# Kernel tuning notes

Measured on AMD Instinct MI355X. Metric: run time of the kernel, lower is better.

## Reference

```python
import jax, jax.numpy as jnp
import numpy as np
from itertools import product

D = 128        # input voxel grid side
N_IN = 150000  # active input voxels
C_IN = 32
C_OUT = 64
M = 100000     # active output voxels kept after stride-2 downsample
EPS = 1e-5


def _build_rulebooks():
    rng = np.random.default_rng(0)
    flat = rng.choice(D ** 3, size=N_IN, replace=False)
    coords = np.stack(np.unravel_index(flat, (D, D, D)), axis=1).astype(np.int64)  # [N_IN,3]
    # SparseConv3d(kernel=2, stride=2, padding=1): input i contributes to output o with
    # i = 2*o - 1 + k, k in {0,1}; per dim exactly one k is valid -> o = (i+1)//2.
    out_all = (coords + 1) // 2
    koff = (coords + 1) % 2
    kidx = koff[:, 0] * 4 + koff[:, 1] * 2 + koff[:, 2]
    out_coords, inv = np.unique(out_all, axis=0, return_inverse=True)
    assert len(out_coords) >= M, 'not enough occupied parent voxels'
    out_coords = out_coords[:M]
    nbr_down = -np.ones((M, 8), np.int32)
    sel = inv < M
    nbr_down[inv[sel], kidx[sel]] = np.arange(N_IN, dtype=np.int32)[sel]
    # SubMConv3d(kernel=3, padding=1): output sites == input sites; neighbor table per offset.
    S = 67  # hash stride (out coords in [0,65), +1 shift keeps neighbor keys in range)
    key = (out_coords[:, 0] + 1) * S * S + (out_coords[:, 1] + 1) * S + (out_coords[:, 2] + 1)
    lut = -np.ones(S ** 3, np.int32)
    lut[key] = np.arange(M, dtype=np.int32)
    nbr_sub = np.empty((M, 27), np.int32)
    for k, (dx, dy, dz) in enumerate(product((-1, 0, 1), repeat=3)):
        nbr_sub[:, k] = lut[key + dx * S * S + dy * S + dz]
    return nbr_down, nbr_sub


def setup_inputs() -> dict:
    nbr_down, nbr_sub = _build_rulebooks()
    key = jax.random.key(0)
    k0, k1, k2, k3, k4 = jax.random.split(key, 5)
    ones = jnp.ones((C_OUT,), jnp.float32)
    zeros = jnp.zeros((C_OUT,), jnp.float32)
    return {
        'x_feats': jax.random.normal(k0, (N_IN, C_IN), jnp.float32),
        'w_down': jax.random.normal(k1, (8, C_IN, C_OUT), jnp.float32) / np.sqrt(8 * C_IN),
        'g_down': ones, 'b_down': zeros,
        'w_proj': jax.random.normal(k2, (C_OUT, C_OUT), jnp.float32) / np.sqrt(C_OUT),
        'g_p': ones, 'b_p': zeros,
        'w1': jax.random.normal(k3, (27, C_OUT, C_OUT), jnp.float32) / np.sqrt(27 * C_OUT),
        'g1': ones, 'b1': zeros,
        'w2': jax.random.normal(k4, (27, C_OUT, C_OUT), jnp.float32) / np.sqrt(27 * C_OUT),
        'g2': ones, 'b2': zeros,
        'nbr_down': jnp.asarray(nbr_down),
        'nbr_sub': jnp.asarray(nbr_sub),
    }


def _bn(f, g, b):
    # BatchNorm1d in training mode over the active-voxel dim (biased variance)
    m = f.mean(0)
    v = jnp.mean((f - m) ** 2, 0)
    return (f - m) * jax.lax.rsqrt(v + EPS) * g + b


def _spconv(feats, nbr, W):
    # rulebook gather-GEMM-scatter: out[m] = sum_k feats[nbr[m,k]] @ W[k]  (nbr=-1 -> zero)
    n = feats.shape[0]
    fpad = jnp.concatenate([feats, jnp.zeros((1, feats.shape[1]), feats.dtype)], axis=0)
    idx = jnp.where(nbr < 0, n, nbr)
    out = jnp.zeros((nbr.shape[0], W.shape[2]), feats.dtype)
    for k in range(W.shape[0]):  # fixed small kernel volume (8 or 27)
        out = out + fpad[idx[:, k]] @ W[k]
    return out


def reference(x_feats, w_down, g_down, b_down, w_proj, g_p, b_p,
              w1, g1, b1, w2, g2, b2, nbr_down, nbr_sub):
    # DonwBlock.down: SparseConv3d -> BN -> ReLU
    x = jax.nn.relu(_bn(_spconv(x_feats, nbr_down, w_down), g_down, b_down))
    # DoubleConv.proj: 1x1 SubMConv (plain linear on features) -> BN
    res = _bn(x @ w_proj, g_p, b_p)
    # conv1 -> bn1 -> relu -> conv2 -> bn2 -> +proj -> relu
    out = jax.nn.relu(_bn(_spconv(x, nbr_sub, w1), g1, b1))
    out = _bn(_spconv(out, nbr_sub, w2), g2, b2) + res
    return jax.nn.relu(out)
```

## Files before the change

### kernel.cpp

```cpp
#include <hip/hip_runtime.h>

static constexpr int M_ROWS = 100000;
static constexpr int N_IN   = 150000;
static constexpr int C_IN   = 32;
static constexpr int CO     = 64;
static constexpr float EPS  = 1e-5f;

typedef __bf16 bf16x8 __attribute__((ext_vector_type(8)));
typedef float  f32x4  __attribute__((ext_vector_type(4)));
typedef unsigned short u16x8 __attribute__((ext_vector_type(8)));
typedef short  short8 __attribute__((ext_vector_type(8)));
typedef unsigned int u32;

static __device__ __forceinline__ unsigned short f2bf(float f) {
    unsigned int u = __builtin_bit_cast(unsigned int, f);
    u += 0x7fff + ((u >> 16) & 1);
    return (unsigned short)(u >> 16);
}
static __device__ __forceinline__ float bf2f(unsigned short h) {
    unsigned int u = ((unsigned int)h) << 16;
    return __builtin_bit_cast(float, u);
}

static __device__ __forceinline__ void gload_lds16(const void* g, void* l) {
    __builtin_amdgcn_global_load_lds(
        (const __attribute__((address_space(1))) u32*)g,
        (__attribute__((address_space(3))) u32*)l, 16, 0, 0);
}

__global__ __launch_bounds__(256) void cvt_bf16(
    const float* __restrict__ in, unsigned short* __restrict__ out, int n8)
{
    int i = blockIdx.x * 256 + threadIdx.x;
    if (i >= n8) return;
    float4 a = ((const float4*)in)[2 * i];
    float4 b = ((const float4*)in)[2 * i + 1];
    u16x8 v;
    v[0] = f2bf(a.x); v[1] = f2bf(a.y); v[2] = f2bf(a.z); v[3] = f2bf(a.w);
    v[4] = f2bf(b.x); v[5] = f2bf(b.y); v[6] = f2bf(b.z); v[7] = f2bf(b.w);
    ((u16x8*)out)[i] = v;
}

__global__ __launch_bounds__(256) void wt_cvt_swz(
    const float* __restrict__ W, unsigned short* __restrict__ WT, int total, int cin)
{
    int t = blockIdx.x * 256 + threadIdx.x;
    if (t >= total) return;
    int k  = t / (cin * 64);
    int r  = t - k * (cin * 64);
    int ci = r >> 6;
    int co = r & 63;
    int xm = (cin == 64) ? ((co & 7) << 4) : ((co & 3) << 4);
    int phys = co * (cin * 2) + ((ci * 2) ^ xm);
    WT[(size_t)k * cin * 64 + (phys >> 1)] = f2bf(W[t]);
}

template<int CIN, int KOFF, int ST, bool GATHER, bool OUTBF>
__global__ __launch_bounds__(256, 2) void spconv_mfma(
    const unsigned short* __restrict__ fB,
    int nZero,
    const int*   __restrict__ nbr,
    const unsigned short* __restrict__ WTs,
    void* __restrict__ outp,
    float* __restrict__ part)
{
    constexpr int KS    = CIN / 32;
    constexpr int SLAB  = CIN * 64;
    constexpr int REPS  = (SLAB * 2) / 4096;
    constexpr int ROWSB = 4 * ST * 16;

    __shared__ unsigned short Wl[2][SLAB];
    __shared__ int nbrS[GATHER ? ROWSB * KOFF : 4];
    __shared__ float red[4][2][64];

    const int tid  = threadIdx.x;
    const int lane = tid & 63;
    const int wv   = tid >> 6;
    const int colb = lane & 15;
    const int kgrp = lane >> 4;

    const int nwg = gridDim.x;
    const int q   = nwg >> 3, r8 = nwg & 7;
    const int xcd = blockIdx.x & 7, pos = blockIdx.x >> 3;
    const int wg  = (xcd < r8 ? xcd * (q + 1) : r8 * (q + 1) + (xcd - r8) * q) + pos;
    const int m0  = wg * ROWSB;

    auto stageW = [&](int k, int b) {
        const unsigned short* g = WTs + (size_t)k * SLAB;
        #pragma unroll
        for (int r = 0; r < REPS; ++r) {
            const void* gp = g + (size_t)(r * 256 + tid) * 8;
            void* lp = &Wl[b][(size_t)(r * 256 + wv * 64) * 8];
            gload_lds16(gp, lp);
        }
    };

    stageW(0, 0);
    if (GATHER) {
        const int* src = nbr + (size_t)m0 * KOFF;
        constexpr int TOT = ROWSB * KOFF;
        if (m0 + ROWSB <= M_ROWS) {
            #pragma unroll 1
            for (int i = tid; i < TOT / 4; i += 256)
                ((int4*)nbrS)[i] = ((const int4*)src)[i];
        } else {
            #pragma unroll 1
            for (int i = tid; i < TOT; i += 256) {
                int r = i / KOFF;
                nbrS[i] = (m0 + r < M_ROWS) ? src[i] : -1;
            }
        }
    }
    __syncthreads();

    auto gatherA = [&](int k, bf16x8 (&dst)[ST][KS]) {
        #pragma unroll
        for (int st = 0; st < ST; ++st) {
            int rloc = wv * (ST * 16) + st * 16 + colb;
            int idx;
            if (GATHER) idx = nbrS[rloc * KOFF + k];
            else        idx = (m0 + rloc < M_ROWS) ? (m0 + rloc) : -1;
            if (idx < 0) idx = nZero;
            const unsigned short* fp = fB + (size_t)idx * CIN + kgrp * 8;
            #pragma unroll
            for (int s = 0; s < KS; ++s)
                dst[st][s] = *reinterpret_cast<const bf16x8*>(fp + s * 32);
        }
    };

    f32x4 acc[ST][4] = {};

    auto compute = [&](int buf, const bf16x8 (&a)[ST][KS]) {
        bf16x8 w[4][KS];
        const char* base = (const char*)&Wl[0][0] + (size_t)buf * SLAB * 2;
        #pragma unroll
        for (int n = 0; n < 4; ++n) {
            int r  = n * 16 + colb;
            int xm = (CIN == 64) ? ((r & 7) << 4) : ((r & 3) << 4);
            #pragma unroll
            for (int s = 0; s < KS; ++s) {
                int c2 = kgrp * 16 + s * 64;
                int phys = r * (CIN * 2) + (c2 ^ xm);
                w[n][s] = *reinterpret_cast<const bf16x8*>(base + phys);
            }
        }
        #pragma unroll
        for (int st = 0; st < ST; ++st)
            #pragma unroll
            for (int n = 0; n < 4; ++n)
                #pragma unroll
                for (int s = 0; s < KS; ++s)
                    acc[st][n] = __builtin_amdgcn_mfma_f32_16x16x32_bf16(
                        a[st][s], w[n][s], acc[st][n], 0, 0, 0);
    };

    #pragma unroll 1
    for (int k = 0; k < KOFF; ++k) {
        bf16x8 a[ST][KS];
        gatherA(k, a);
        if (k + 1 < KOFF) stageW(k + 1, (k + 1) & 1);
        compute(k & 1, a);
        if (k + 1 < KOFF) __syncthreads();
    }

    #pragma unroll
    for (int st = 0; st < ST; ++st) {
        int rbase = m0 + wv * (ST * 16) + st * 16 + kgrp * 4;
        #pragma unroll
        for (int j = 0; j < 4; ++j) {
            int row = rbase + j;
            if (row < M_ROWS) {
                if (OUTBF) {
                    unsigned short* o = (unsigned short*)outp;
                    #pragma unroll
                    for (int n = 0; n < 4; ++n)
                        o[(size_t)row * 64 + n * 16 + colb] = f2bf(acc[st][n][j]);
                } else {
                    float* o = (float*)outp;
                    #pragma unroll
                    for (int n = 0; n < 4; ++n)
                        o[(size_t)row * 64 + n * 16 + colb] = acc[st][n][j];
                }
            }
        }
    }

    float s4[4], q4[4];
    #pragma unroll
    for (int n = 0; n < 4; ++n) {
        float s = 0.f, qq = 0.f;
        #pragma unroll
        for (int st = 0; st < ST; ++st)
            #pragma unroll
            for (int j = 0; j < 4; ++j) {
                float v = acc[st][n][j];
                s += v; qq += v * v;
            }
        s4[n] = s; q4[n] = qq;
    }
    #pragma unroll
    for (int n = 0; n < 4; ++n) {
        s4[n] += __shfl_xor(s4[n], 16); s4[n] += __shfl_xor(s4[n], 32);
        q4[n] += __shfl_xor(q4[n], 16); q4[n] += __shfl_xor(q4[n], 32);
    }
    if (kgrp == 0) {
        #pragma unroll
        for (int n = 0; n < 4; ++n) {
            red[wv][0][n * 16 + colb] = s4[n];
            red[wv][1][n * 16 + colb] = q4[n];
        }
    }
    __syncthreads();
    if (tid < 64) {
        float S = red[0][0][tid] + red[1][0][tid] + red[2][0][tid] + red[3][0][tid];
        float Q = red[0][1][tid] + red[1][1][tid] + red[2][1][tid] + red[3][1][tid];
        part[(size_t)wg * 128 + tid]      = S;
        part[(size_t)wg * 128 + 64 + tid] = Q;
    }
}

__global__ __launch_bounds__(1024) void bn_finalize(
    const float* __restrict__ part, int nblocks,
    const float* __restrict__ gg, const float* __restrict__ bb,
    float* __restrict__ ss, int M)
{
    const int tid = threadIdx.x;
    const int c   = tid & 63;
    const int grp = tid >> 6;
    float S = 0.f, Q = 0.f;
    int i = grp;
    for (; i + 48 < nblocks; i += 64) {
        float a0 = part[(size_t)(i     ) * 128 + c];
        float a1 = part[(size_t)(i + 16) * 128 + c];
        float a2 = part[(size_t)(i + 32) * 128 + c];
        float a3 = part[(size_t)(i + 48) * 128 + c];
        float q0 = part[(size_t)(i     ) * 128 + 64 + c];
        float q1 = part[(size_t)(i + 16) * 128 + 64 + c];
        float q2 = part[(size_t)(i + 32) * 128 + 64 + c];
        float q3 = part[(size_t)(i + 48) * 128 + 64 + c];
        S += a0 + a1 + a2 + a3;
        Q += q0 + q1 + q2 + q3;
    }
    for (; i < nblocks; i += 16) {
        S += part[(size_t)i * 128 + c];
        Q += part[(size_t)i * 128 + 64 + c];
    }
    __shared__ float sh[2][16][64];
    sh[0][grp][c] = S; sh[1][grp][c] = Q;
    __syncthreads();
    if (tid < 64) {
        float Sa = 0.f, Qa = 0.f;
        #pragma unroll
        for (int j = 0; j < 16; ++j) { Sa += sh[0][j][tid]; Qa += sh[1][j][tid]; }
        float mean = Sa / (float)M;
        float var  = Qa / (float)M - mean * mean;
        float rstd = rsqrtf(var + EPS);
        float sc = gg[tid] * rstd;
        ss[tid]      = sc;
        ss[64 + tid] = bb[tid] - mean * sc;
    }
}

template<bool INBF, bool BF16OUT, bool RES, bool RELU>
__global__ __launch_bounds__(256) void bn_apply(
    const void* __restrict__ yp, const float* __restrict__ ss,
    const unsigned short* __restrict__ res, void* __restrict__ out, int n8)
{
    for (int i = blockIdx.x * 256 + threadIdx.x; i < n8; i += gridDim.x * 256) {
        float v[8];
        if (INBF) {
            u16x8 u = ((const u16x8*)yp)[i];
            #pragma unroll
            for (int j = 0; j < 8; ++j) v[j] = bf2f(u[j]);
        } else {
            float4 a = ((const float4*)yp)[2 * i];
            float4 b = ((const float4*)yp)[2 * i + 1];
            v[0] = a.x; v[1] = a.y; v[2] = a.z; v[3] = a.w;
            v[4] = b.x; v[5] = b.y; v[6] = b.z; v[7] = b.w;
        }
        int c0 = (i * 8) & 63;
        #pragma unroll
        for (int j = 0; j < 8; ++j)
            v[j] = v[j] * ss[c0 + j] + ss[64 + c0 + j];
        if (RES) {
            u16x8 rv = ((const u16x8*)res)[i];
            #pragma unroll
            for (int j = 0; j < 8; ++j) v[j] += bf2f(rv[j]);
        }
        if (RELU) {
            #pragma unroll
            for (int j = 0; j < 8; ++j) v[j] = fmaxf(v[j], 0.f);
        }
        if (BF16OUT) {
            u16x8 o;
            #pragma unroll
            for (int j = 0; j < 8; ++j) o[j] = f2bf(v[j]);
            ((u16x8*)out)[i] = o;
        } else {
            float4 oa, ob;
            oa.x = v[0]; oa.y = v[1]; oa.z = v[2]; oa.w = v[3];
            ob.x = v[4]; ob.y = v[5]; ob.z = v[6]; ob.w = v[7];
            ((float4*)out)[2 * i]     = oa;
            ((float4*)out)[2 * i + 1] = ob;
        }
    }
}

extern "C" void kernel_launch(void* const* d_in, const int* in_sizes, int n_in,
                              void* d_out, int out_size, void* d_ws, size_t ws_size,
                              hipStream_t stream)
{
    const float* x_feats = (const float*)d_in[0];
    const float* w_down  = (const float*)d_in[1];
    const float* g_down  = (const float*)d_in[2];
    const float* b_down  = (const float*)d_in[3];
    const float* w_proj  = (const float*)d_in[4];
    const float* g_p     = (const float*)d_in[5];
    const float* b_p     = (const float*)d_in[6];
    const float* w1      = (const float*)d_in[7];
    const float* g1      = (const float*)d_in[8];
    const float* b1      = (const float*)d_in[9];
    const float* w2      = (const float*)d_in[10];
    const float* g2      = (const float*)d_in[11];
    const float* b2      = (const float*)d_in[12];
    const int*   nbr_down = (const int*)d_in[13];
    const int*   nbr_sub  = (const int*)d_in[14];
    float* out = (float*)d_out;

    const int M = M_ROWS;
    const int conv_grid = (M + 255) / 256;
    const size_t feat4 = (size_t)M * CO * 4;
    const size_t feat2 = (size_t)(M + 1) * CO * 2;
    auto align = [](size_t x) { return (x + 255) & ~(size_t)255; };

    char* ws = (char*)d_ws;
    size_t off = 0;
    unsigned short* xin16 = (unsigned short*)(ws + off); off += align((size_t)(N_IN + 1) * C_IN * 2);
    unsigned short* wdT   = (unsigned short*)(ws + off); off += align((size_t)8 * CO * C_IN * 2);
    unsigned short* wpT   = (unsigned short*)(ws + off); off += align((size_t)1 * CO * CO * 2);
    unsigned short* w1T   = (unsigned short*)(ws + off); off += align((size_t)27 * CO * CO * 2);
    unsigned short* w2T   = (unsigned short*)(ws + off); off += align((size_t)27 * CO * CO * 2);
    float* Y    = (float*)(ws + off); off += align(feat4);
    unsigned short* bufRb = (unsigned short*)(ws + off); off += align(feat2);
    unsigned short* xB = (unsigned short*)(ws + off); off += align(feat2);
    unsigned short* zB = (unsigned short*)(ws + off); off += align(feat2);
    float* part = (float*)(ws + off); off += align((size_t)1024 * 128 * 4);
    float* ss0  = (float*)(ws + off);
    float* ss1  = ss0 + 128;
    float* ss2  = ss1 + 128;
    float* ss3  = ss2 + 128;

    unsigned short* Yb = (unsigned short*)Y;

    const int n8 = M * CO / 8;
    const int ew_grid = 2048;

    hipMemsetAsync(xin16 + (size_t)N_IN * C_IN, 0, C_IN * 2, stream);
    hipMemsetAsync(xB + (size_t)M * CO, 0, CO * 2, stream);
    hipMemsetAsync(zB + (size_t)M * CO, 0, CO * 2, stream);

    {
        int nf8 = N_IN * C_IN / 8;
        cvt_bf16<<<(nf8 + 255) / 256, 256, 0, stream>>>(x_feats, xin16, nf8);
        int t;
        t = 8 * C_IN * CO;  wt_cvt_swz<<<(t + 255) / 256, 256, 0, stream>>>(w_down, wdT, t, C_IN);
        t = CO * CO;        wt_cvt_swz<<<(t + 255) / 256, 256, 0, stream>>>(w_proj, wpT, t, CO);
        t = 27 * CO * CO;   wt_cvt_swz<<<(t + 255) / 256, 256, 0, stream>>>(w1, w1T, t, CO);
        t = 27 * CO * CO;   wt_cvt_swz<<<(t + 255) / 256, 256, 0, stream>>>(w2, w2T, t, CO);
    }

    spconv_mfma<C_IN, 8, 4, true, true><<<conv_grid, 256, 0, stream>>>(
        xin16, N_IN, nbr_down, wdT, Yb, part);
    bn_finalize<<<1, 1024, 0, stream>>>(part, conv_grid, g_down, b_down, ss0, M);
    bn_apply<true, true, false, true><<<ew_grid, 256, 0, stream>>>(Yb, ss0, nullptr, xB, n8);

    spconv_mfma<CO, 1, 4, false, true><<<conv_grid, 256, 0, stream>>>(
        xB, M, nullptr, wpT, Yb, part);
    bn_finalize<<<1, 1024, 0, stream>>>(part, conv_grid, g_p, b_p, ss1, M);
    bn_apply<true, true, false, false><<<ew_grid, 256, 0, stream>>>(Yb, ss1, nullptr, bufRb, n8);

    spconv_mfma<CO, 27, 4, true, true><<<conv_grid, 256, 0, stream>>>(
        xB, M, nbr_sub, w1T, Yb, part);
    bn_finalize<<<1, 1024, 0, stream>>>(part, conv_grid, g1, b1, ss2, M);
    bn_apply<true, true, false, true><<<ew_grid, 256, 0, stream>>>(Yb, ss2, nullptr, zB, n8);

    spconv_mfma<CO, 27, 4, true, false><<<conv_grid, 256, 0, stream>>>(
        zB, M, nbr_sub, w2T, Y, part);
    bn_finalize<<<1, 1024, 0, stream>>>(part, conv_grid, g2, b2, ss3, M);
    bn_apply<false, false, true, true><<<ew_grid, 256, 0, stream>>>(Y, ss3, bufRb, out, n8);
}
```

Before: 182.3 us.

## Use 512-thread conv blocks, fuse weight conversions, store last conv output as bf16

The sparse conv kernel now runs with 512 threads (8 waves) per 256-row block and ST fixed at 2, where before it used 4 waves with ST=4. Weight staging is now done by a subset of waves. The four weight-conversion launches are merged into one kernel, removing launch overhead. The final conv also writes bf16 instead of fp32, halving that intermediate's traffic at the cost of slightly lower precision before the last batch norm.

```diff
diff --git a/kernel.cpp b/kernel.cpp
--- a/kernel.cpp
+++ b/kernel.cpp
@@ -41,22 +41,30 @@
     ((u16x8*)out)[i] = v;
 }
 
-__global__ __launch_bounds__(256) void wt_cvt_swz(
-    const float* __restrict__ W, unsigned short* __restrict__ WT, int total, int cin)
+__global__ __launch_bounds__(256) void wt_cvt_all(
+    const float* __restrict__ wd, const float* __restrict__ wp,
+    const float* __restrict__ w1, const float* __restrict__ w2,
+    unsigned short* __restrict__ wdT, unsigned short* __restrict__ wpT,
+    unsigned short* __restrict__ w1T, unsigned short* __restrict__ w2T)
 {
     int t = blockIdx.x * 256 + threadIdx.x;
-    if (t >= total) return;
-    int k  = t / (cin * 64);
-    int r  = t - k * (cin * 64);
+    if (t >= 241664) return;
+    const float* W; unsigned short* WT; int cin, tt;
+    if (t < 16384)       { W = wd; WT = wdT; cin = 32; tt = t; }
+    else if (t < 20480)  { W = wp; WT = wpT; cin = 64; tt = t - 16384; }
+    else if (t < 131072) { W = w1; WT = w1T; cin = 64; tt = t - 20480; }
+    else                 { W = w2; WT = w2T; cin = 64; tt = t - 131072; }
+    int k  = tt / (cin * 64);
+    int r  = tt - k * (cin * 64);
     int ci = r >> 6;
     int co = r & 63;
     int xm = (cin == 64) ? ((co & 7) << 4) : ((co & 3) << 4);
     int phys = co * (cin * 2) + ((ci * 2) ^ xm);
-    WT[(size_t)k * cin * 64 + (phys >> 1)] = f2bf(W[t]);
-}
-
-template<int CIN, int KOFF, int ST, bool GATHER, bool OUTBF>
-__global__ __launch_bounds__(256, 2) void spconv_mfma(
+    WT[(size_t)k * cin * 64 + (phys >> 1)] = f2bf(W[tt]);
+}
+
+template<int CIN, int KOFF, bool GATHER, bool OUTBF>
+__global__ __launch_bounds__(512) void spconv_mfma(
     const unsigned short* __restrict__ fB,
     int nZero,
     const int*   __restrict__ nbr,
@@ -64,14 +72,15 @@
     void* __restrict__ outp,
     float* __restrict__ part)
 {
-    constexpr int KS    = CIN / 32;
-    constexpr int SLAB  = CIN * 64;
-    constexpr int REPS  = (SLAB * 2) / 4096;
-    constexpr int ROWSB = 4 * ST * 16;
+    constexpr int KS     = CIN / 32;
+    constexpr int ST     = 2;
+    constexpr int ROWS   = 256;
+    constexpr int SLAB   = CIN * 64;
+    constexpr int SWAVES = CIN / 8;
 
     __shared__ unsigned short Wl[2][SLAB];
-    __shared__ int nbrS[GATHER ? ROWSB * KOFF : 4];
-    __shared__ float red[4][2][64];
+    __shared__ int nbrS[GATHER ? ROWS * KOFF : 4];
+    __shared__ float red[8][2][64];
 
     const int tid  = threadIdx.x;
     const int lane = tid & 63;
@@ -83,14 +92,12 @@
     const int q   = nwg >> 3, r8 = nwg & 7;
     const int xcd = blockIdx.x & 7, pos = blockIdx.x >> 3;
     const int wg  = (xcd < r8 ? xcd * (q + 1) : r8 * (q + 1) + (xcd - r8) * q) + pos;
-    const int m0  = wg * ROWSB;
+    const int m0  = wg * ROWS;
 
     auto stageW = [&](int k, int b) {
-        const unsigned short* g = WTs + (size_t)k * SLAB;
-        #pragma unroll
-        for (int r = 0; r < REPS; ++r) {
-            const void* gp = g + (size_t)(r * 256 + tid) * 8;
-            void* lp = &Wl[b][(size_t)(r * 256 + wv * 64) * 8];
+        if (wv < SWAVES) {
+            const unsigned short* gp = WTs + (size_t)k * SLAB + wv * 512 + lane * 8;
+            void* lp = &Wl[b][wv * 512];
             gload_lds16(gp, lp);
         }
     };
@@ -98,14 +105,14 @@
     stageW(0, 0);
     if (GATHER) {
         const int* src = nbr + (size_t)m0 * KOFF;
-        constexpr int TOT = ROWSB * KOFF;
-        if (m0 + ROWSB <= M_ROWS) {
+        constexpr int TOT = ROWS * KOFF;
+        if (m0 + ROWS <= M_ROWS) {
             #pragma unroll 1
-            for (int i = tid; i < TOT / 4; i += 256)
+            for (int i = tid; i < TOT / 4; i += 512)
                 ((int4*)nbrS)[i] = ((const int4*)src)[i];
         } else {
             #pragma unroll 1
-            for (int i = tid; i < TOT; i += 256) {
+            for (int i = tid; i < TOT; i += 512) {
                 int r = i / KOFF;
                 nbrS[i] = (m0 + r < M_ROWS) ? src[i] : -1;
             }
@@ -212,8 +219,9 @@
     }
     __syncthreads();
     if (tid < 64) {
-        float S = red[0][0][tid] + red[1][0][tid] + red[2][0][tid] + red[3][0][tid];
-        float Q = red[0][1][tid] + red[1][1][tid] + red[2][1][tid] + red[3][1][tid];
+        float S = 0.f, Q = 0.f;
+        #pragma unroll
+        for (int w8 = 0; w8 < 8; ++w8) { S += red[w8][0][tid]; Q += red[w8][1][tid]; }
         part[(size_t)wg * 128 + tid]      = S;
         part[(size_t)wg * 128 + 64 + tid] = Q;
     }
@@ -329,7 +337,6 @@
 
     const int M = M_ROWS;
     const int conv_grid = (M + 255) / 256;
-    const size_t feat4 = (size_t)M * CO * 4;
     const size_t feat2 = (size_t)(M + 1) * CO * 2;
     auto align = [](size_t x) { return (x + 255) & ~(size_t)255; };
 
@@ -340,18 +347,16 @@
     unsigned short* wpT   = (unsigned short*)(ws + off); off += align((size_t)1 * CO * CO * 2);
     unsigned short* w1T   = (unsigned short*)(ws + off); off += align((size_t)27 * CO * CO * 2);
     unsigned short* w2T   = (unsigned short*)(ws + off); off += align((size_t)27 * CO * CO * 2);
-    float* Y    = (float*)(ws + off); off += align(feat4);
+    unsigned short* Yb    = (unsigned short*)(ws + off); off += align(feat2);
     unsigned short* bufRb = (unsigned short*)(ws + off); off += align(feat2);
-    unsigned short* xB = (unsigned short*)(ws + off); off += align(feat2);
-    unsigned short* zB = (unsigned short*)(ws + off); off += align(feat2);
+    unsigned short* xB    = (unsigned short*)(ws + off); off += align(feat2);
+    unsigned short* zB    = (unsigned short*)(ws + off); off += align(feat2);
     float* part = (float*)(ws + off); off += align((size_t)1024 * 128 * 4);
     float* ss0  = (float*)(ws + off);
     float* ss1  = ss0 + 128;
     float* ss2  = ss1 + 128;
     float* ss3  = ss2 + 128;
 
-    unsigned short* Yb = (unsigned short*)Y;
-
     const int n8 = M * CO / 8;
     const int ew_grid = 2048;
 
@@ -362,30 +367,27 @@
     {
         int nf8 = N_IN * C_IN / 8;
         cvt_bf16<<<(nf8 + 255) / 256, 256, 0, stream>>>(x_feats, xin16, nf8);
-        int t;
-        t = 8 * C_IN * CO;  wt_cvt_swz<<<(t + 255) / 256, 256, 0, stream>>>(w_down, wdT, t, C_IN);
-        t = CO * CO;        wt_cvt_swz<<<(t + 255) / 256, 256, 0, stream>>>(w_proj, wpT, t, CO);
-        t = 27 * CO * CO;   wt_cvt_swz<<<(t + 255) / 256, 256, 0, stream>>>(w1, w1T, t, CO);
-        t = 27 * CO * CO;   wt_cvt_swz<<<(t + 255) / 256, 256, 0, stream>>>(w2, w2T, t, CO);
-    }
-
-    spconv_mfma<C_IN, 8, 4, true, true><<<conv_grid, 256, 0, stream>>>(
+        wt_cvt_all<<<(241664 + 255) / 256, 256, 0, stream>>>(
+            w_down, w_proj, w1, w2, wdT, wpT, w1T, w2T);
+    }
+
+    spconv_mfma<C_IN, 8, true, true><<<conv_grid, 512, 0, stream>>>(
         xin16, N_IN, nbr_down, wdT, Yb, part);
     bn_finalize<<<1, 1024, 0, stream>>>(part, conv_grid, g_down, b_down, ss0, M);
     bn_apply<true, true, false, true><<<ew_grid, 256, 0, stream>>>(Yb, ss0, nullptr, xB, n8);
 
-    spconv_mfma<CO, 1, 4, false, true><<<conv_grid, 256, 0, stream>>>(
+    spconv_mfma<CO, 1, false, true><<<conv_grid, 512, 0, stream>>>(
         xB, M, nullptr, wpT, Yb, part);
     bn_finalize<<<1, 1024, 0, stream>>>(part, conv_grid, g_p, b_p, ss1, M);
     bn_apply<true, true, false, false><<<ew_grid, 256, 0, stream>>>(Yb, ss1, nullptr, bufRb, n8);
 
-    spconv_mfma<CO, 27, 4, true, true><<<conv_grid, 256, 0, stream>>>(
+    spconv_mfma<CO, 27, true, true><<<conv_grid, 512, 0, stream>>>(
         xB, M, nbr_sub, w1T, Yb, part);
     bn_finalize<<<1, 1024, 0, stream>>>(part, conv_grid, g1, b1, ss2, M);
     bn_apply<true, true, false, true><<<ew_grid, 256, 0, stream>>>(Yb, ss2, nullptr, zB, n8);
 
-    spconv_mfma<CO, 27, 4, true, false><<<conv_grid, 256, 0, stream>>>(
-        zB, M, nbr_sub, w2T, Y, part);
+    spconv_mfma<CO, 27, true, true><<<conv_grid, 512, 0, stream>>>(
+        zB, M, nbr_sub, w2T, Yb, part);
     bn_finalize<<<1, 1024, 0, stream>>>(part, conv_grid, g2, b2, ss3, M);
-    bn_apply<false, false, true, true><<<ew_grid, 256, 0, stream>>>(Y, ss3, bufRb, out, n8);
-}
+    bn_apply<true, false, true, true><<<ew_grid, 256, 0, stream>>>(Yb, ss3, bufRb, out, n8);
+}
```

After: 171.7 us. 1.06x faster.
